# Performance work log

Measured on AMD Instinct MI355X. Metric: run time of the kernel, lower is better.

Reference implementation:

```python
import jax, jax.numpy as jnp
import numpy as np

MODEL_DIM = 1024
NUM_HEADS = 16
HEAD_DIM = MODEL_DIM // NUM_HEADS
ROPE_THETA = 10000.0


def _rotate_half(x):
    x1, x2 = jnp.split(x, 2, axis=-1)
    return jnp.concatenate((-x2, x1), axis=-1)


def _rope_cos_sin(seq_len, dtype):
    inv_freq = 1.0 / (ROPE_THETA ** (jnp.arange(0, HEAD_DIM, 2, dtype=jnp.float32) / HEAD_DIM))
    pos = jnp.arange(seq_len, dtype=jnp.float32)
    freqs = jnp.einsum('i,j->ij', pos, inv_freq)  # [S, HEAD_DIM/2]
    emb = jnp.concatenate((freqs, freqs), axis=-1)  # [S, HEAD_DIM]
    return jnp.cos(emb).astype(dtype), jnp.sin(emb).astype(dtype)


def setup_inputs() -> dict:
    key = jax.random.key(0)
    ks = jax.random.split(key, 9)
    B, S, D = 4, 2048, MODEL_DIM
    scale = 1.0 / np.sqrt(D)
    inp = {
        'x': jax.random.normal(ks[0], (B, S, D), dtype=jnp.float32),
        'key_padding_mask': jnp.ones((B, S), dtype=bool),
        'wq': jax.random.normal(ks[1], (D, D), dtype=jnp.float32) * scale,
        'bq': jnp.zeros((D,), dtype=jnp.float32),
        'wk': jax.random.normal(ks[2], (D, D), dtype=jnp.float32) * scale,
        'bk': jnp.zeros((D,), dtype=jnp.float32),
        'wv': jax.random.normal(ks[3], (D, D), dtype=jnp.float32) * scale,
        'bv': jnp.zeros((D,), dtype=jnp.float32),
        'wo': jax.random.normal(ks[4], (D, D), dtype=jnp.float32) * scale,
        'bo': jnp.zeros((D,), dtype=jnp.float32),
    }
    return inp


def reference(x, key_padding_mask, wq, bq, wk, bk, wv, bv, wo, bo):
    B, S, D = x.shape
    H, Hd = NUM_HEADS, HEAD_DIM
    q = (x @ wq + bq).reshape(B, S, H, Hd).transpose(0, 2, 1, 3)
    k = (x @ wk + bk).reshape(B, S, H, Hd).transpose(0, 2, 1, 3)
    v = (x @ wv + bv).reshape(B, S, H, Hd).transpose(0, 2, 1, 3)
    cos, sin = _rope_cos_sin(S, x.dtype)  # [S, Hd]
    cos = cos[None, None]
    sin = sin[None, None]
    q = q * cos + _rotate_half(q) * sin
    k = k * cos + _rotate_half(k) * sin
    scores = jnp.einsum('bhqd,bhkd->bhqk', q, k) / jnp.sqrt(jnp.asarray(Hd, x.dtype))
    mask = key_padding_mask[:, None, None, :]
    scores = jnp.where(mask, scores, jnp.finfo(scores.dtype).min)
    attn = jax.nn.softmax(scores, axis=-1)
    ctx = jnp.einsum('bhqk,bhkd->bhqd', attn, v)
    ctx = ctx.transpose(0, 2, 1, 3).reshape(B, S, D)
    out = ctx @ wo + bo
    out = out * key_padding_mask[:, :, None].astype(out.dtype)
    return out
```

## Files before the change

### kernel.cpp

```cpp
#include <hip/hip_runtime.h>
#include <math.h>

#define S_LEN  2048
#define NH     16
#define HD     64
#define DMODEL 1024
#define BATCH  4
#define M_TOK  (BATCH * S_LEN)

typedef __bf16 bf16x8 __attribute__((ext_vector_type(8)));
typedef float  floatx4 __attribute__((ext_vector_type(4)));
typedef float  floatx16 __attribute__((ext_vector_type(16)));

typedef __attribute__((address_space(1))) const void cg_void;
typedef __attribute__((address_space(3))) void lds_void;

#if __has_builtin(__builtin_amdgcn_exp2f)
#define EXP2(x) __builtin_amdgcn_exp2f(x)
#else
#define EXP2(x) exp2f(x)
#endif

__device__ __forceinline__ void gload16(const void* g, void* l) {
    __builtin_amdgcn_global_load_lds((cg_void*)g, (lds_void*)l, 16, 0, 0);
}

__device__ __forceinline__ unsigned short f2bf(float f) {
    unsigned int u = __builtin_bit_cast(unsigned int, f);
    u = (u + 0x7FFF + ((u >> 16) & 1)) >> 16;
    return (unsigned short)u;
}

__device__ __forceinline__ unsigned cvtpk(float lo, float hi) {
    unsigned r;
    asm volatile("v_cvt_pk_bf16_f32 %0, %1, %2" : "=v"(r) : "v"(lo), "v"(hi));
    return r;
}

__device__ __forceinline__ void swap32(unsigned &a, unsigned &b) {
    asm volatile("v_permlane32_swap_b32 %0, %1" : "+v"(a), "+v"(b));
}

__device__ __forceinline__ float max3f(float a, float b, float c) {
    float r;
    asm("v_max3_f32 %0, %1, %2, %3" : "=v"(r) : "v"(a), "v"(b), "v"(c));
    return r;
}

__global__ __launch_bounds__(256)
void prep_kernel(const float* __restrict__ x,
                 const float* __restrict__ wq, const float* __restrict__ wk,
                 const float* __restrict__ wv, const float* __restrict__ wo,
                 const int* __restrict__ mask,
                 unsigned short* __restrict__ xb, unsigned short* __restrict__ wstack,
                 unsigned short* __restrict__ wto,
                 float* __restrict__ cs, float* __restrict__ sn,
                 float* __restrict__ biasG, unsigned* __restrict__ flagmask)
{
    __shared__ float tile[32][33];
    __shared__ unsigned fm[4];
    const int blk = blockIdx.x;
    const int tid = threadIdx.x;
    constexpr size_t WSZ = (size_t)DMODEL * DMODEL;

    if (blk < 8192) {
        const int idx = blk * 256 + tid;
        float4 a = *reinterpret_cast<const float4*>(&x[(size_t)idx * 4]);
        ushort4 o;
        o.x = f2bf(a.x); o.y = f2bf(a.y); o.z = f2bf(a.z); o.w = f2bf(a.w);
        *reinterpret_cast<ushort4*>(&xb[(size_t)idx * 4]) = o;
    } else if (blk < 12288) {
        const int rel = blk - 8192;
        const int mat = rel >> 10;
        const float* w = (mat == 0) ? wq : (mat == 1) ? wk : (mat == 2) ? wv : wo;
        unsigned short* wt = (mat < 3) ? (wstack + (size_t)mat * WSZ) : wto;
        const int rel10 = rel & 1023;
        const int n0 = (rel10 & 31) * 32;
        const int k0 = (rel10 >> 5) * 32;
        const int tx  = tid & 31;
        const int ty8 = tid >> 5;
        #pragma unroll
        for (int i = 0; i < 4; ++i)
            tile[ty8 + i * 8][tx] = w[(size_t)(k0 + ty8 + i * 8) * DMODEL + n0 + tx];
        __syncthreads();
        #pragma unroll
        for (int i = 0; i < 4; ++i)
            wt[(size_t)(n0 + ty8 + i * 8) * DMODEL + k0 + tx] = f2bf(tile[tx][ty8 + i * 8]);
    } else if (blk < 12544) {
        const int idx = (blk - 12288) * 256 + tid;
        const int j = idx & 31;
        const int s = idx >> 5;
        const float invf = exp2f(-(float)j * (13.287712379549449f / 32.0f));
        const float a = (float)s * invf;
        cs[idx] = cosf(a);
        sn[idx] = sinf(a);
    } else {
        for (int i = tid; i < BATCH * S_LEN; i += 256) {
            const int b = i >> 11, r = i & 2047;
            const int kt = r >> 6, rem = r & 63;
            const int hig = rem >> 5, kbb = (rem >> 4) & 1, reg = rem & 15;
            const int key = kt * 64 + kbb * 32 + hig * 4 + (reg & 3) + ((reg >> 2) << 3);
            biasG[i] = mask[b * S_LEN + key] ? 0.0f : -3.0e38f;
        }
        if (tid < 4) fm[tid] = 0;
        __syncthreads();
        for (int i = tid; i < BATCH * 32; i += 256) {
            const int b = i >> 5, kt = i & 31;
            int ok = 1;
            for (int j = 0; j < 64; ++j) ok &= (mask[b * S_LEN + kt * 64 + j] != 0);
            if (ok) atomicOr(&fm[b], 1u << kt);
        }
        __syncthreads();
        if (tid < 4) flagmask[tid] = fm[tid];
    }
}

__global__ __launch_bounds__(256)
void gemm_qkv(const unsigned short* __restrict__ A, const unsigned short* __restrict__ Bt,
              const float* __restrict__ bq, const float* __restrict__ bk,
              const float* __restrict__ bv,
              const float* __restrict__ cs, const float* __restrict__ sn,
              unsigned short* __restrict__ qbf, unsigned short* __restrict__ kbf,
              unsigned short* __restrict__ vtb)
{
    constexpr int K = DMODEL;
    __shared__ unsigned short As[2][128 * 32];
    __shared__ unsigned short Bs[2][128 * 32];

    const int tid  = threadIdx.x;
    const int lane = tid & 63;
    const int w    = tid >> 6;
    const int wm   = w >> 1;
    const int wn   = w & 1;

    const int gx   = gridDim.x;
    int lin = blockIdx.y * gx + blockIdx.x;
    const int cpx = (gx * gridDim.y) >> 3;
    lin = (lin & 7) * cpx + (lin >> 3);
    const int row0 = (lin / gx) * 128;
    const int col0 = (lin % gx) * 128;

    const int sr  = lane >> 2;
    const int sk8 = (lane & 3) * 8;
    const int fr  = lane & 15;
    const int fk  = (lane >> 4) * 8;

    floatx4 acc[4][4] = {};

    #pragma unroll
    for (int t = 0; t < 2; ++t) {
        const int chunk = w * 32 + t * 16;
        gload16(A  + (size_t)(row0 + chunk + sr) * K + sk8, &As[0][chunk * 32]);
        gload16(Bt + (size_t)(col0 + chunk + sr) * K + sk8, &Bs[0][chunk * 32]);
    }

    for (int kt = 0; kt < K / 32; ++kt) {
        __syncthreads();
        if (kt + 1 < K / 32) {
            const int nb = (kt + 1) & 1;
            const int k0 = (kt + 1) * 32;
            #pragma unroll
            for (int t = 0; t < 2; ++t) {
                const int chunk = w * 32 + t * 16;
                gload16(A  + (size_t)(row0 + chunk + sr) * K + k0 + sk8, &As[nb][chunk * 32]);
                gload16(Bt + (size_t)(col0 + chunk + sr) * K + k0 + sk8, &Bs[nb][chunk * 32]);
            }
        }
        const int cur = kt & 1;
        bf16x8 av[4], bv4[4];
        #pragma unroll
        for (int m = 0; m < 4; ++m)
            av[m] = *reinterpret_cast<const bf16x8*>(&As[cur][(wm * 64 + m * 16 + fr) * 32 + fk]);
        #pragma unroll
        for (int n = 0; n < 4; ++n)
            bv4[n] = *reinterpret_cast<const bf16x8*>(&Bs[cur][(wn * 64 + n * 16 + fr) * 32 + fk]);
        #pragma unroll
        for (int m = 0; m < 4; ++m)
            #pragma unroll
            for (int n = 0; n < 4; ++n)
                acc[m][n] = __builtin_amdgcn_mfma_f32_16x16x32_bf16(av[m], bv4[n], acc[m][n], 0, 0, 0);
    }

    const int rbase = lane >> 4;
    const int sect  = col0 >> 10;
    const int c0    = col0 & 1023;

    if (sect == 2) {
        #pragma unroll
        for (int m = 0; m < 4; ++m)
            #pragma unroll
            for (int n = 0; n < 4; ++n) {
                const int c  = c0 + wn * 64 + n * 16 + fr;
                const int hh = c >> 6, d = c & 63;
                const int mr0 = row0 + wm * 64 + m * 16 + rbase * 4;
                const int bb = mr0 >> 11, ss = mr0 & (S_LEN - 1);
                const float bc = bv[c];
                ushort4 pk4;
                pk4.x = f2bf(acc[m][n][0] + bc);
                pk4.y = f2bf(acc[m][n][1] + bc);
                pk4.z = f2bf(acc[m][n][2] + bc);
                pk4.w = f2bf(acc[m][n][3] + bc);
                *reinterpret_cast<ushort4*>(
                    &vtb[((size_t)(bb * NH + hh) * HD + d) * S_LEN + ss]) = pk4;
            }
    } else {
        unsigned short* outp = sect ? kbf : qbf;
        const float* bias = sect ? bk : bq;
        const float sc = sect ? 1.0f : 0.125f * 1.44269504088896f;
        #pragma unroll
        for (int m = 0; m < 4; ++m)
            #pragma unroll
            for (int n = 0; n < 2; ++n) {
                const int c  = c0 + wn * 64 + n * 16 + fr;
                const int hh = c >> 6, d = c & 63;
                const float b1 = bias[c], b2 = bias[c + 32];
                #pragma unroll
                for (int r = 0; r < 4; ++r) {
                    const int mr = row0 + wm * 64 + m * 16 + rbase * 4 + r;
                    const int bb = mr >> 11, ss = mr & (S_LEN - 1);
                    const float v1 = acc[m][n][r] + b1;
                    const float v2 = acc[m][n + 2][r] + b2;
                    const float co = cs[ss * 32 + d];
                    const float si = sn[ss * 32 + d];
                    const size_t base = ((size_t)(bb * NH + hh) * S_LEN + ss) * HD + d;
                    outp[base]      = f2bf((v1 * co - v2 * si) * sc);
                    outp[base + 32] = f2bf((v2 * co + v1 * si) * sc);
                }
            }
    }
}

__global__ __launch_bounds__(512)
void attn_mfma3(const unsigned short* __restrict__ qbf,
                const unsigned short* __restrict__ kbf,
                const unsigned short* __restrict__ vtb,
                const float* __restrict__ biasG,
                const unsigned* __restrict__ flagmask,
                unsigned short* __restrict__ ctxb)
{
    __shared__ unsigned short Ks[4][64 * 64];
    __shared__ unsigned short Vs[4][64 * 64];

    const int tid  = threadIdx.x;
    const int lane = tid & 63;
    const int w    = tid >> 6;
    const int bh   = blockIdx.x;
    const int b    = bh >> 4;
    const int h    = bh & 15;
    const int q0   = blockIdx.y * 256 + w * 32;
    const size_t hb = (size_t)bh * S_LEN * HD;

    const int lo5 = lane & 31;
    const int hi5 = lane >> 5;
    const int srow   = lane >> 3;
    const int schunk = (lane & 7) ^ srow;
    const unsigned fl = flagmask[b];

    bf16x8 qf[4];
    #pragma unroll
    for (int ks = 0; ks < 4; ++ks)
        qf[ks] = *reinterpret_cast<const bf16x8*>(
            &qbf[hb + (size_t)(q0 + lo5) * HD + ks * 16 + hi5 * 8]);

    floatx16 oacc[2];
    #pragma unroll
    for (int v = 0; v < 2; ++v)
        #pragma unroll
        for (int i = 0; i < 16; ++i) oacc[v][i] = 0.0f;
    float mrow = -3.0e38f, lrow = 0.0f;

    #define STAGE(KT, BUF) do {                                                             \
        const int r0 = w * 8;                                                               \
        gload16(kbf + hb + (size_t)((KT) * 64 + r0 + srow) * HD + schunk * 8,               \
                &Ks[BUF][r0 * 64]);                                                         \
        gload16(vtb + ((size_t)bh * HD + r0 + srow) * S_LEN + (KT) * 64 + schunk * 8,       \
                &Vs[BUF][r0 * 64]);                                                         \
    } while (0)

    auto TILE = [&](int kt, int buf) {
        floatx16 sacc[2];
        if ((fl >> kt) & 1u) {
            #pragma unroll
            for (int kb = 0; kb < 2; ++kb)
                #pragma unroll
                for (int i = 0; i < 16; ++i) sacc[kb][i] = 0.0f;
        } else {
            const float4* bp = reinterpret_cast<const float4*>(
                &biasG[(size_t)(b * 32 + kt) * 64 + hi5 * 32]);
            #pragma unroll
            for (int kb = 0; kb < 2; ++kb)
                #pragma unroll
                for (int t = 0; t < 4; ++t) {
                    const float4 b4 = bp[kb * 4 + t];
                    sacc[kb][t * 4 + 0] = b4.x; sacc[kb][t * 4 + 1] = b4.y;
                    sacc[kb][t * 4 + 2] = b4.z; sacc[kb][t * 4 + 3] = b4.w;
                }
        }

        __builtin_amdgcn_s_setprio(1);
        #pragma unroll
        for (int kb = 0; kb < 2; ++kb) {
            #pragma unroll
            for (int ks = 0; ks < 4; ++ks) {
                const bf16x8 ak = *reinterpret_cast<const bf16x8*>(
                    (const char*)&Ks[buf][0] + (kb * 32 + lo5) * 128 +
                    ((ks * 32 + hi5 * 16) ^ ((lo5 & 7) << 4)));
                sacc[kb] = __builtin_amdgcn_mfma_f32_32x32x16_bf16(ak, qf[ks], sacc[kb], 0, 0, 0);
            }
        }
        __builtin_amdgcn_s_setprio(0);

        float r0 = max3f(sacc[0][0],  sacc[0][1],  sacc[0][2]);
        float r1 = max3f(sacc[0][3],  sacc[0][4],  sacc[0][5]);
        float r2 = max3f(sacc[0][6],  sacc[0][7],  sacc[0][8]);
        float r3 = max3f(sacc[0][9],  sacc[0][10], sacc[0][11]);
        float r4 = max3f(sacc[0][12], sacc[0][13], sacc[0][14]);
        float r5 = max3f(sacc[1][0],  sacc[1][1],  sacc[1][2]);
        float r6 = max3f(sacc[1][3],  sacc[1][4],  sacc[1][5]);
        float r7 = max3f(sacc[1][6],  sacc[1][7],  sacc[1][8]);
        float r8 = max3f(sacc[1][9],  sacc[1][10], sacc[1][11]);
        float r9 = max3f(sacc[1][12], sacc[1][13], sacc[1][14]);
        float s1 = max3f(r0, r1, r2);
        float s2 = max3f(r3, r4, r5);
        float s3 = max3f(r6, r7, r8);
        float s4 = max3f(r9, sacc[0][15], sacc[1][15]);
        float pmax = fmaxf(max3f(s1, s2, s3), s4);
        pmax = fmaxf(pmax, __shfl_xor(pmax, 32));

        if (!__all(pmax <= mrow + 8.0f)) {
            const float mnew = fmaxf(mrow, pmax);
            const float fscale = EXP2(mrow - mnew);
            mrow = mnew;
            lrow *= fscale;
            #pragma unroll
            for (int v = 0; v < 2; ++v)
                #pragma unroll
                for (int i = 0; i < 16; ++i) oacc[v][i] *= fscale;
        }

        float rs0 = 0.0f, rs1 = 0.0f, rs2 = 0.0f, rs3 = 0.0f;
        #pragma unroll
        for (int kb = 0; kb < 2; ++kb)
            #pragma unroll
            for (int i = 0; i < 16; i += 4) {
                float p0 = EXP2(sacc[kb][i + 0] - mrow);
                float p1 = EXP2(sacc[kb][i + 1] - mrow);
                float p2 = EXP2(sacc[kb][i + 2] - mrow);
                float p3 = EXP2(sacc[kb][i + 3] - mrow);
                sacc[kb][i + 0] = p0; sacc[kb][i + 1] = p1;
                sacc[kb][i + 2] = p2; sacc[kb][i + 3] = p3;
                rs0 += p0; rs1 += p1; rs2 += p2; rs3 += p3;
            }
        float rs = (rs0 + rs1) + (rs2 + rs3);
        rs += __shfl_xor(rs, 32);
        lrow += rs;

        unsigned U0[8], U1[8];
        #pragma unroll
        for (int kb = 0; kb < 2; ++kb)
            #pragma unroll
            for (int s = 0; s < 4; ++s) {
                U0[kb * 4 + s] = cvtpk(sacc[kb][4 * s + 0], sacc[kb][4 * s + 1]);
                U1[kb * 4 + s] = cvtpk(sacc[kb][4 * s + 2], sacc[kb][4 * s + 3]);
            }
        union PF { unsigned u[4]; bf16x8 v; };
        PF pf[4];
        #pragma unroll
        for (int ks = 0; ks < 4; ++ks) {
            unsigned a0 = U0[2 * ks], b0 = U0[2 * ks + 1];
            swap32(a0, b0);
            unsigned a1 = U1[2 * ks], b1 = U1[2 * ks + 1];
            swap32(a1, b1);
            pf[ks].u[0] = a0; pf[ks].u[1] = a1;
            pf[ks].u[2] = b0; pf[ks].u[3] = b1;
        }

        __builtin_amdgcn_s_setprio(1);
        #pragma unroll
        for (int vb = 0; vb < 2; ++vb) {
            #pragma unroll
            for (int ks = 0; ks < 4; ++ks) {
                const bf16x8 av = *reinterpret_cast<const bf16x8*>(
                    (const char*)&Vs[buf][0] + (vb * 32 + lo5) * 128 +
                    ((ks * 32 + hi5 * 16) ^ ((lo5 & 7) << 4)));
                oacc[vb] = __builtin_amdgcn_mfma_f32_32x32x16_bf16(av, pf[ks].v, oacc[vb], 0, 0, 0);
            }
        }
        __builtin_amdgcn_s_setprio(0);
    };

    STAGE(0, 0);
    STAGE(1, 1);

    for (int kt = 0; kt < 30; ++kt) {
        STAGE(kt + 2, (kt + 2) & 3);
        asm volatile("s_waitcnt vmcnt(4)" ::: "memory");
        __builtin_amdgcn_s_barrier();
        __builtin_amdgcn_sched_barrier(0);
        TILE(kt, kt & 3);
    }
    asm volatile("s_waitcnt vmcnt(2)" ::: "memory");
    __builtin_amdgcn_s_barrier();
    __builtin_amdgcn_sched_barrier(0);
    TILE(30, 30 & 3);
    asm volatile("s_waitcnt vmcnt(0)" ::: "memory");
    __builtin_amdgcn_s_barrier();
    __builtin_amdgcn_sched_barrier(0);
    TILE(31, 31 & 3);

    const float inv = 1.0f / lrow;
    unsigned short* dst = &ctxb[((size_t)b * S_LEN + q0 + lo5) * DMODEL + h * HD];
    #pragma unroll
    for (int vb = 0; vb < 2; ++vb)
        #pragma unroll
        for (int s = 0; s < 4; ++s) {
            const int d0 = vb * 32 + s * 8 + hi5 * 4;
            ushort4 o4;
            o4.x = f2bf(oacc[vb][4 * s + 0] * inv);
            o4.y = f2bf(oacc[vb][4 * s + 1] * inv);
            o4.z = f2bf(oacc[vb][4 * s + 2] * inv);
            o4.w = f2bf(oacc[vb][4 * s + 3] * inv);
            *reinterpret_cast<ushort4*>(&dst[d0]) = o4;
        }
    #undef STAGE
}

__global__ __launch_bounds__(256)
void gemm_out(const unsigned short* __restrict__ A, const unsigned short* __restrict__ Bt,
              const float* __restrict__ bias, const int* __restrict__ mask,
              float* __restrict__ C)
{
    constexpr int K = DMODEL;
    __shared__ unsigned short As[2][128 * 32];
    __shared__ unsigned short Bs[2][128 * 32];

    const int tid  = threadIdx.x;
    const int lane = tid & 63;
    const int w    = tid >> 6;
    const int wm   = w >> 1;
    const int wn   = w & 1;

    const int gx   = gridDim.x;
    int lin = blockIdx.y * gx + blockIdx.x;
    const int cpx = (gx * gridDim.y) >> 3;
    lin = (lin & 7) * cpx + (lin >> 3);
    const int row0 = (lin >> 3) * 128;
    const int col0 = (lin & 7) * 128;

    const int sr  = lane >> 2;
    const int sk8 = (lane & 3) * 8;
    const int fr  = lane & 15;
    const int fk  = (lane >> 4) * 8;

    floatx4 acc[4][4] = {};

    #pragma unroll
    for (int t = 0; t < 2; ++t) {
        const int chunk = w * 32 + t * 16;
        gload16(A  + (size_t)(row0 + chunk + sr) * K + sk8, &As[0][chunk * 32]);
        gload16(Bt + (size_t)(col0 + chunk + sr) * K + sk8, &Bs[0][chunk * 32]);
    }

    for (int kt = 0; kt < K / 32; ++kt) {
        __syncthreads();
        if (kt + 1 < K / 32) {
            const int nb = (kt + 1) & 1;
            const int k0 = (kt + 1) * 32;
            #pragma unroll
            for (int t = 0; t < 2; ++t) {
                const int chunk = w * 32 + t * 16;
                gload16(A  + (size_t)(row0 + chunk + sr) * K + k0 + sk8, &As[nb][chunk * 32]);
                gload16(Bt + (size_t)(col0 + chunk + sr) * K + k0 + sk8, &Bs[nb][chunk * 32]);
            }
        }
        const int cur = kt & 1;
        bf16x8 av[4], bv4[4];
        #pragma unroll
        for (int m = 0; m < 4; ++m)
            av[m] = *reinterpret_cast<const bf16x8*>(&As[cur][(wm * 64 + m * 16 + fr) * 32 + fk]);
        #pragma unroll
        for (int n = 0; n < 4; ++n)
            bv4[n] = *reinterpret_cast<const bf16x8*>(&Bs[cur][(wn * 64 + n * 16 + fr) * 32 + fk]);
        #pragma unroll
        for (int m = 0; m < 4; ++m)
            #pragma unroll
            for (int n = 0; n < 4; ++n)
                acc[m][n] = __builtin_amdgcn_mfma_f32_16x16x32_bf16(av[m], bv4[n], acc[m][n], 0, 0, 0);
    }

    const int rbase = lane >> 4;
    #pragma unroll
    for (int m = 0; m < 4; ++m)
        #pragma unroll
        for (int n = 0; n < 4; ++n) {
            const int c = col0 + wn * 64 + n * 16 + fr;
            const float bc = bias[c];
            #pragma unroll
            for (int r = 0; r < 4; ++r) {
                const int mr = row0 + wm * 64 + m * 16 + rbase * 4 + r;
                C[(size_t)mr * DMODEL + c] = mask[mr] ? (acc[m][n][r] + bc) : 0.0f;
            }
        }
}

extern "C" void kernel_launch(void* const* d_in, const int* in_sizes, int n_in,
                              void* d_out, int out_size, void* d_ws, size_t ws_size,
                              hipStream_t stream) {
    const float* x    = (const float*)d_in[0];
    const int*   mask = (const int*)d_in[1];
    const float* wq = (const float*)d_in[2];
    const float* bq = (const float*)d_in[3];
    const float* wk = (const float*)d_in[4];
    const float* bk = (const float*)d_in[5];
    const float* wv = (const float*)d_in[6];
    const float* bv = (const float*)d_in[7];
    const float* wo = (const float*)d_in[8];
    const float* bo = (const float*)d_in[9];
    float* out = (float*)d_out;

    const size_t QKV = (size_t)M_TOK * DMODEL;
    const size_t WSZ = (size_t)DMODEL * DMODEL;
    unsigned short* xb     = (unsigned short*)d_ws;
    unsigned short* wstack = xb + QKV;
    unsigned short* wto    = wstack + 3 * WSZ;
    unsigned short* qbf    = wto + WSZ;
    unsigned short* kbf    = qbf + QKV;
    unsigned short* vtb    = kbf + QKV;
    unsigned short* ctxb   = vtb + QKV;
    float* cs    = (float*)(ctxb + QKV);
    float* sn    = cs + (size_t)S_LEN * 32;
    float* biasG = sn + (size_t)S_LEN * 32;
    unsigned* flagmask = (unsigned*)(biasG + (size_t)BATCH * S_LEN);

    prep_kernel<<<12545, 256, 0, stream>>>(x, wq, wk, wv, wo, mask,
                                           xb, wstack, wto, cs, sn, biasG, flagmask);

    dim3 qkvgrid(3 * DMODEL / 128, M_TOK / 128);
    gemm_qkv<<<qkvgrid, 256, 0, stream>>>(xb, wstack, bq, bk, bv, cs, sn, qbf, kbf, vtb);

    dim3 agrid(BATCH * NH, S_LEN / 256);
    attn_mfma3<<<agrid, 512, 0, stream>>>(qbf, kbf, vtb, biasG, flagmask, ctxb);

    dim3 ogrid(DMODEL / 128, M_TOK / 128);
    gemm_out<<<ogrid, 256, 0, stream>>>(ctxb, wto, bo, mask, out);
}
```

Measured before the change: 309.8 us.

## Deepen GEMM LDS pipeline to four buffers with prefetch distance two

```diff
diff --git a/kernel.cpp b/kernel.cpp
--- a/kernel.cpp
+++ b/kernel.cpp
@@ -94,7 +94,7 @@
         const float a = (float)s * invf;
         cs[idx] = cosf(a);
         sn[idx] = sinf(a);
-    } else {
+    } else if (blk == 12544) {
         for (int i = tid; i < BATCH * S_LEN; i += 256) {
             const int b = i >> 11, r = i & 2047;
             const int kt = r >> 6, rem = r & 63;
@@ -102,6 +102,7 @@
             const int key = kt * 64 + kbb * 32 + hig * 4 + (reg & 3) + ((reg >> 2) << 3);
             biasG[i] = mask[b * S_LEN + key] ? 0.0f : -3.0e38f;
         }
+    } else {
         if (tid < 4) fm[tid] = 0;
         __syncthreads();
         for (int i = tid; i < BATCH * 32; i += 256) {
@@ -124,8 +125,8 @@
               unsigned short* __restrict__ vtb)
 {
     constexpr int K = DMODEL;
-    __shared__ unsigned short As[2][128 * 32];
-    __shared__ unsigned short Bs[2][128 * 32];
+    __shared__ unsigned short As[4][128 * 32];
+    __shared__ unsigned short Bs[4][128 * 32];
 
     const int tid  = threadIdx.x;
     const int lane = tid & 63;
@@ -147,39 +148,51 @@
 
     floatx4 acc[4][4] = {};
 
-    #pragma unroll
-    for (int t = 0; t < 2; ++t) {
-        const int chunk = w * 32 + t * 16;
-        gload16(A  + (size_t)(row0 + chunk + sr) * K + sk8, &As[0][chunk * 32]);
-        gload16(Bt + (size_t)(col0 + chunk + sr) * K + sk8, &Bs[0][chunk * 32]);
-    }
-
-    for (int kt = 0; kt < K / 32; ++kt) {
-        __syncthreads();
-        if (kt + 1 < K / 32) {
-            const int nb = (kt + 1) & 1;
-            const int k0 = (kt + 1) * 32;
-            #pragma unroll
-            for (int t = 0; t < 2; ++t) {
-                const int chunk = w * 32 + t * 16;
-                gload16(A  + (size_t)(row0 + chunk + sr) * K + k0 + sk8, &As[nb][chunk * 32]);
-                gload16(Bt + (size_t)(col0 + chunk + sr) * K + k0 + sk8, &Bs[nb][chunk * 32]);
-            }
-        }
-        const int cur = kt & 1;
+    #define GSTAGE(KT, BUF) do {                                                            \
+        const int k0_ = (KT) * 32;                                                          \
+        _Pragma("unroll")                                                                   \
+        for (int t = 0; t < 2; ++t) {                                                       \
+            const int chunk = w * 32 + t * 16;                                              \
+            gload16(A  + (size_t)(row0 + chunk + sr) * K + k0_ + sk8, &As[BUF][chunk * 32]);\
+            gload16(Bt + (size_t)(col0 + chunk + sr) * K + k0_ + sk8, &Bs[BUF][chunk * 32]);\
+        }                                                                                   \
+    } while (0)
+
+    auto COMPUTE = [&](int buf) {
         bf16x8 av[4], bv4[4];
         #pragma unroll
         for (int m = 0; m < 4; ++m)
-            av[m] = *reinterpret_cast<const bf16x8*>(&As[cur][(wm * 64 + m * 16 + fr) * 32 + fk]);
+            av[m] = *reinterpret_cast<const bf16x8*>(&As[buf][(wm * 64 + m * 16 + fr) * 32 + fk]);
         #pragma unroll
         for (int n = 0; n < 4; ++n)
-            bv4[n] = *reinterpret_cast<const bf16x8*>(&Bs[cur][(wn * 64 + n * 16 + fr) * 32 + fk]);
+            bv4[n] = *reinterpret_cast<const bf16x8*>(&Bs[buf][(wn * 64 + n * 16 + fr) * 32 + fk]);
+        __builtin_amdgcn_s_setprio(1);
         #pragma unroll
         for (int m = 0; m < 4; ++m)
             #pragma unroll
             for (int n = 0; n < 4; ++n)
                 acc[m][n] = __builtin_amdgcn_mfma_f32_16x16x32_bf16(av[m], bv4[n], acc[m][n], 0, 0, 0);
+        __builtin_amdgcn_s_setprio(0);
+    };
+
+    GSTAGE(0, 0);
+    GSTAGE(1, 1);
+    for (int kt = 0; kt < 30; ++kt) {
+        GSTAGE(kt + 2, (kt + 2) & 3);
+        asm volatile("s_waitcnt vmcnt(8)" ::: "memory");
+        __builtin_amdgcn_s_barrier();
+        __builtin_amdgcn_sched_barrier(0);
+        COMPUTE(kt & 3);
     }
+    asm volatile("s_waitcnt vmcnt(4)" ::: "memory");
+    __builtin_amdgcn_s_barrier();
+    __builtin_amdgcn_sched_barrier(0);
+    COMPUTE(2);
+    asm volatile("s_waitcnt vmcnt(0)" ::: "memory");
+    __builtin_amdgcn_s_barrier();
+    __builtin_amdgcn_sched_barrier(0);
+    COMPUTE(3);
+    #undef GSTAGE
 
     const int rbase = lane >> 4;
     const int sect  = col0 >> 10;
@@ -212,7 +225,7 @@
             #pragma unroll
             for (int n = 0; n < 2; ++n) {
                 const int c  = c0 + wn * 64 + n * 16 + fr;
-                const int hh = c >> 6, d = c & 63;
+                const int hh = c >> 6, dd = c & 63;
                 const float b1 = bias[c], b2 = bias[c + 32];
                 #pragma unroll
                 for (int r = 0; r < 4; ++r) {
@@ -220,11 +233,13 @@
                     const int bb = mr >> 11, ss = mr & (S_LEN - 1);
                     const float v1 = acc[m][n][r] + b1;
                     const float v2 = acc[m][n + 2][r] + b2;
-                    const float co = cs[ss * 32 + d];
-                    const float si = sn[ss * 32 + d];
-                    const size_t base = ((size_t)(bb * NH + hh) * S_LEN + ss) * HD + d;
-                    outp[base]      = f2bf((v1 * co - v2 * si) * sc);
-                    outp[base + 32] = f2bf((v2 * co + v1 * si) * sc);
+                    const float co = cs[ss * 32 + dd];
+                    const float si = sn[ss * 32 + dd];
+                    ushort2 st;
+                    st.x = f2bf((v1 * co - v2 * si) * sc);
+                    st.y = f2bf((v2 * co + v1 * si) * sc);
+                    *reinterpret_cast<ushort2*>(
+                        &outp[((size_t)(bb * NH + hh) * S_LEN + ss) * HD + 2 * dd]) = st;
                 }
             }
     }
@@ -431,8 +446,8 @@
               float* __restrict__ C)
 {
     constexpr int K = DMODEL;
-    __shared__ unsigned short As[2][128 * 32];
-    __shared__ unsigned short Bs[2][128 * 32];
+    __shared__ unsigned short As[4][128 * 32];
+    __shared__ unsigned short Bs[4][128 * 32];
 
     const int tid  = threadIdx.x;
     const int lane = tid & 63;
@@ -454,39 +469,51 @@
 
     floatx4 acc[4][4] = {};
 
-    #pragma unroll
-    for (int t = 0; t < 2; ++t) {
-        const int chunk = w * 32 + t * 16;
-        gload16(A  + (size_t)(row0 + chunk + sr) * K + sk8, &As[0][chunk * 32]);
-        gload16(Bt + (size_t)(col0 + chunk + sr) * K + sk8, &Bs[0][chunk * 32]);
-    }
-
-    for (int kt = 0; kt < K / 32; ++kt) {
-        __syncthreads();
-        if (kt + 1 < K / 32) {
-            const int nb = (kt + 1) & 1;
-            const int k0 = (kt + 1) * 32;
-            #pragma unroll
-            for (int t = 0; t < 2; ++t) {
-                const int chunk = w * 32 + t * 16;
-                gload16(A  + (size_t)(row0 + chunk + sr) * K + k0 + sk8, &As[nb][chunk * 32]);
-                gload16(Bt + (size_t)(col0 + chunk + sr) * K + k0 + sk8, &Bs[nb][chunk * 32]);
-            }
-        }
-        const int cur = kt & 1;
+    #define GSTAGE(KT, BUF) do {                                                            \
+        const int k0_ = (KT) * 32;                                                          \
+        _Pragma("unroll")                                                                   \
+        for (int t = 0; t < 2; ++t) {                                                       \
+            const int chunk = w * 32 + t * 16;                                              \
+            gload16(A  + (size_t)(row0 + chunk + sr) * K + k0_ + sk8, &As[BUF][chunk * 32]);\
+            gload16(Bt + (size_t)(col0 + chunk + sr) * K + k0_ + sk8, &Bs[BUF][chunk * 32]);\
+        }                                                                                   \
+    } while (0)
+
+    auto COMPUTE = [&](int buf) {
         bf16x8 av[4], bv4[4];
         #pragma unroll
         for (int m = 0; m < 4; ++m)
-            av[m] = *reinterpret_cast<const bf16x8*>(&As[cur][(wm * 64 + m * 16 + fr) * 32 + fk]);
+            av[m] = *reinterpret_cast<const bf16x8*>(&As[buf][(wm * 64 + m * 16 + fr) * 32 + fk]);
         #pragma unroll
         for (int n = 0; n < 4; ++n)
-            bv4[n] = *reinterpret_cast<const bf16x8*>(&Bs[cur][(wn * 64 + n * 16 + fr) * 32 + fk]);
+            bv4[n] = *reinterpret_cast<const bf16x8*>(&Bs[buf][(wn * 64 + n * 16 + fr) * 32 + fk]);
+        __builtin_amdgcn_s_setprio(1);
         #pragma unroll
         for (int m = 0; m < 4; ++m)
             #pragma unroll
             for (int n = 0; n < 4; ++n)
                 acc[m][n] = __builtin_amdgcn_mfma_f32_16x16x32_bf16(av[m], bv4[n], acc[m][n], 0, 0, 0);
+        __builtin_amdgcn_s_setprio(0);
+    };
+
+    GSTAGE(0, 0);
+    GSTAGE(1, 1);
+    for (int kt = 0; kt < 30; ++kt) {
+        GSTAGE(kt + 2, (kt + 2) & 3);
+        asm volatile("s_waitcnt vmcnt(8)" ::: "memory");
+        __builtin_amdgcn_s_barrier();
+        __builtin_amdgcn_sched_barrier(0);
+        COMPUTE(kt & 3);
     }
+    asm volatile("s_waitcnt vmcnt(4)" ::: "memory");
+    __builtin_amdgcn_s_barrier();
+    __builtin_amdgcn_sched_barrier(0);
+    COMPUTE(2);
+    asm volatile("s_waitcnt vmcnt(0)" ::: "memory");
+    __builtin_amdgcn_s_barrier();
+    __builtin_amdgcn_sched_barrier(0);
+    COMPUTE(3);
+    #undef GSTAGE
 
     const int rbase = lane >> 4;
     #pragma unroll
@@ -532,7 +559,7 @@
     float* biasG = sn + (size_t)S_LEN * 32;
     unsigned* flagmask = (unsigned*)(biasG + (size_t)BATCH * S_LEN);
 
-    prep_kernel<<<12545, 256, 0, stream>>>(x, wq, wk, wv, wo, mask,
+    prep_kernel<<<12546, 256, 0, stream>>>(x, wq, wk, wv, wo, mask,
                                            xb, wstack, wto, cs, sn, biasG, flagmask);
 
     dim3 qkvgrid(3 * DMODEL / 128, M_TOK / 128);
```

Result: faster. 291.3 us (-6.0%).
